# Optimization experiments

Measured on AMD Instinct MI355X. Metric: run time of the kernel, lower is better.

The kernel has to match this reference:

```python
import jax, jax.numpy as jnp
import numpy as np

B, T, DIN, E, H, P = 8, 2048, 256, 256, 4, 8
HD = E // H


def _xavier(key, out_dim, in_dim):
    lim = float(np.sqrt(6.0 / (in_dim + out_dim)))
    return jax.random.uniform(key, (out_dim, in_dim), jnp.float32, -lim, lim)


def setup_inputs() -> dict:
    key = jax.random.key(0)
    ks = jax.random.split(key, 9)
    return {
        "x": jax.random.normal(ks[0], (B, T, DIN), jnp.float32),
        "w_in": _xavier(ks[1], E, DIN), "b_in": jnp.zeros((E,), jnp.float32),
        # MHA in-projections (torch packs qkv; xavier over packed [3E,E] approximated per-slice)
        "w_q": _xavier(ks[2], E, E), "b_q": jnp.zeros((E,), jnp.float32),
        "w_k": _xavier(ks[3], E, E), "b_k": jnp.zeros((E,), jnp.float32),
        "w_v": _xavier(ks[4], E, E), "b_v": jnp.zeros((E,), jnp.float32),
        "w_o": _xavier(ks[5], E, E), "b_o": jnp.zeros((E,), jnp.float32),
        "w_bd": _xavier(ks[6], 1, E), "b_bd": jnp.zeros((1,), jnp.float32),
        "w_pr": _xavier(ks[7], E, E), "b_pr": jnp.zeros((E,), jnp.float32),
    }


def reference(x, w_in, b_in, w_q, b_q, w_k, b_k, w_v, b_v, w_o, b_o, w_bd, b_bd, w_pr, b_pr):
    b, t, _ = x.shape
    h = x @ w_in.T + b_in                                   # [B,T,E]
    # self-attention (batch_first MHA, eval mode -> dropout is identity)
    q = (h @ w_q.T + b_q).reshape(b, t, H, HD)
    k = (h @ w_k.T + b_k).reshape(b, t, H, HD)
    v = (h @ w_v.T + b_v).reshape(b, t, H, HD)
    scale = 1.0 / np.sqrt(HD).astype(np.float32)
    scores = jnp.einsum("bqhd,bkhd->bhqk", q * scale, k)   # [B,H,T,T]
    attn = jax.nn.softmax(scores, axis=-1)
    ao = jnp.einsum("bhqk,bkhd->bqhd", attn, v).reshape(b, t, E)
    ao = ao @ w_o.T + b_o
    # boundary scoring -> dynamic patch ids
    bs = jax.nn.sigmoid(ao @ w_bd.T + b_bd)[..., 0]         # [B,T]
    cum = jnp.cumsum(bs, axis=1)
    normalized = cum / jnp.maximum(cum[:, -1:], 1e-6)
    pid = jnp.minimum((normalized * P).astype(jnp.int32), P - 1)  # [B,T]
    # mean-pool h into P dynamic patches (scatter_add + counts, via one-hot segment matmul)
    oh = jax.nn.one_hot(pid, P, dtype=h.dtype)              # [B,T,P]
    patch_emb = jnp.einsum("btp,btd->bpd", oh, h)           # [B,P,E]
    counts = oh.sum(axis=1)[..., None]                      # [B,P,1]
    patch_emb = patch_emb / jnp.maximum(counts, 1.0)
    return patch_emb @ w_pr.T + b_pr                        # [B,P,E]
```

## Files before the change

kernel.cpp:

```cpp
#include <hip/hip_runtime.h>
#include <cstddef>

#define NB 8
#define NT 2048
#define NE 256
#define NH 4
#define ND 64
#define NP 8

typedef short bf16x8 __attribute__((ext_vector_type(8)));
typedef float f32x4 __attribute__((ext_vector_type(4)));

__device__ __forceinline__ unsigned short f2bf(float f) {
  unsigned u = __builtin_bit_cast(unsigned, f);
  u += 0x7fffu + ((u >> 16) & 1u);
  return (unsigned short)(u >> 16);
}
__device__ __forceinline__ float bf2f(unsigned short h) {
  unsigned u = ((unsigned)h) << 16;
  return __builtin_bit_cast(float, u);
}
__device__ __forceinline__ void split2(float a, float b, unsigned& hi, unsigned& lo) {
  const unsigned short ha = f2bf(a), hb = f2bf(b);
  hi = (unsigned)ha | ((unsigned)hb << 16);
  const unsigned short la = f2bf(a - bf2f(ha));
  const unsigned short lb = f2bf(b - bf2f(hb));
  lo = (unsigned)la | ((unsigned)lb << 16);
}
__device__ __forceinline__ void gld16(const void* g, void* l) {
  __builtin_amdgcn_global_load_lds((const __attribute__((address_space(1))) unsigned*)g,
                                   (__attribute__((address_space(3))) unsigned*)l, 16, 0, 0);
}

__global__ __launch_bounds__(256) void setup_kernel(
    const float* __restrict__ w_in, const float* __restrict__ w_q,
    const float* __restrict__ w_k, const float* __restrict__ b_q,
    const float* __restrict__ b_k, const float* __restrict__ w_o,
    const float* __restrict__ b_o, const float* __restrict__ w_bd,
    const float* __restrict__ b_bd, const float* __restrict__ w_v,
    const float* __restrict__ b_v,
    unsigned short* __restrict__ wihi, unsigned short* __restrict__ wilo,
    unsigned short* __restrict__ wqkvhi, unsigned short* __restrict__ wqkvlo,
    float* __restrict__ bqk, float* __restrict__ consts, float* __restrict__ psum)
{
  __shared__ float wbd_s[NE];
  __shared__ float u_s[NE];
  const int b = blockIdx.x, tid = threadIdx.x;
  if (b < 512) {
    const int i = b * 256 + tid;
    const float v = (i < 65536) ? w_q[i] * 0.125f : w_k[i - 65536];
    const unsigned short h = f2bf(v);
    wqkvhi[i] = h;
    wqkvlo[i] = f2bf(v - bf2f(h));
    if (i < 512) bqk[i] = (i < 256) ? b_q[i] * 0.125f : b_k[i - 256];
  } else if (b < 576) {
    const int i = (b - 512) * 256 + tid;
    const float4 v = *(const float4*)(w_in + (size_t)i * 4);
    const float vv[4] = {v.x, v.y, v.z, v.w};
    unsigned short h4[4], l4[4];
    #pragma unroll
    for (int j = 0; j < 4; ++j) {
      h4[j] = f2bf(vv[j]);
      l4[j] = f2bf(vv[j] - bf2f(h4[j]));
    }
    *(ushort2*)(wihi + (size_t)i * 4)     = make_ushort2(h4[0], h4[1]);
    *(ushort2*)(wihi + (size_t)i * 4 + 2) = make_ushort2(h4[2], h4[3]);
    *(ushort2*)(wilo + (size_t)i * 4)     = make_ushort2(l4[0], l4[1]);
    *(ushort2*)(wilo + (size_t)i * 4 + 2) = make_ushort2(l4[2], l4[3]);
  } else if (b == 576) {
    wbd_s[tid] = w_bd[tid];
    __syncthreads();
    float a = 0.f;
    for (int j = 0; j < NE; ++j) a = fmaf(wbd_s[j], w_o[j * NE + tid], a);
    u_s[tid] = a;
    __syncthreads();
    #pragma unroll
    for (int hh = 0; hh < NH; ++hh) {
      float a2 = 0.f;
      for (int d = 0; d < ND; ++d)
        a2 = fmaf(u_s[hh * ND + d], w_v[(size_t)(hh * ND + d) * NE + tid], a2);
      const unsigned short hb = f2bf(a2);
      wqkvhi[(512 + hh) * 256 + tid] = hb;
      wqkvlo[(512 + hh) * 256 + tid] = f2bf(a2 - bf2f(hb));
    }
    for (int i = tid; i < 60 * 256; i += 256) {
      wqkvhi[516 * 256 + i] = 0;
      wqkvlo[516 * 256 + i] = 0;
    }
    if (tid == 0) {
      float cc = 0.f;
      for (int j = 0; j < NE; ++j) cc = fmaf(wbd_s[j], b_o[j], cc);
      consts[0] = cc + b_bd[0];
    }
    if (tid < 4) {
      float cv = 0.f;
      for (int d = 0; d < ND; ++d) cv = fmaf(u_s[tid * ND + d], b_v[tid * ND + d], cv);
      bqk[512 + tid] = cv;
    } else if (tid < 64) {
      bqk[512 + tid] = 0.f;
    }
  } else {
    for (int i = tid; i < NB * NP * NE; i += 256) psum[i] = 0.f;
  }
}

__global__ __launch_bounds__(256) void hgemm_kernel(
    const float* __restrict__ x,
    const unsigned short* __restrict__ wihi, const unsigned short* __restrict__ wilo,
    const float* __restrict__ b_in,
    unsigned short* __restrict__ hhi, unsigned short* __restrict__ hlo)
{
  __shared__ __align__(16) char sm[2][24576];
  const int tid = threadIdx.x;
  const int wave = tid >> 6, lane = tid & 63;
  const int lr = lane & 15, lg = lane >> 4;
  const int wm = wave >> 1, wn = wave & 1;
  const int bid = blockIdx.x;
  const int idx = bid >> 3;
  const int m0 = ((bid & 7) * 16 + (idx >> 2)) * 128;
  const int n0 = (idx & 3) * 64;

  const float* aSrc[4];
  #pragma unroll
  for (int c = 0; c < 4; ++c) {
    const int L = c * 4096 + tid * 16;
    const int row = L >> 7, w = (L >> 4) & 7;
    aSrc[c] = x + (size_t)(m0 + row) * 256 + (w ^ (row & 7)) * 4;
  }
  const unsigned short* wSrc[2];
  #pragma unroll
  for (int c = 0; c < 2; ++c) {
    const int L = c * 4096 + tid * 16;
    const int half = (L >> 12) & 1;
    const int Lh = L & 4095;
    const int col = Lh >> 6, w = (Lh >> 4) & 3;
    wSrc[c] = (half ? wilo : wihi) + (size_t)(n0 + col) * 256 + (w ^ ((col >> 1) & 3)) * 8;
  }
  int aoff[4][2], woff[2];
  #pragma unroll
  for (int s = 0; s < 4; ++s) {
    const int row = wm * 64 + s * 16 + lr;
    const int b0 = row * 128 + lg * 32;
    const int f = (row & 7) << 4;
    aoff[s][0] = b0 ^ f;
    aoff[s][1] = (b0 + 16) ^ f;
  }
  #pragma unroll
  for (int ns = 0; ns < 2; ++ns) {
    const int col = wn * 32 + ns * 16 + lr;
    woff[ns] = (col * 64 + lg * 16) ^ (((col >> 1) & 3) << 4);
  }

  f32x4 acc[4][2];
  #pragma unroll
  for (int s = 0; s < 4; ++s)
    #pragma unroll
    for (int ns = 0; ns < 2; ++ns) acc[s][ns] = (f32x4){0.f, 0.f, 0.f, 0.f};

  {
    char* lb = sm[0];
    #pragma unroll
    for (int c = 0; c < 4; ++c) gld16(aSrc[c], lb + c * 4096 + wave * 1024);
    #pragma unroll
    for (int c = 0; c < 2; ++c) gld16(wSrc[c], lb + 16384 + c * 4096 + wave * 1024);
  }

  for (int kt = 0; kt < 8; ++kt) {
    __syncthreads();
    if (kt < 7) {
      char* nb = sm[(kt + 1) & 1];
      #pragma unroll
      for (int c = 0; c < 4; ++c) gld16(aSrc[c] + (kt + 1) * 32, nb + c * 4096 + wave * 1024);
      #pragma unroll
      for (int c = 0; c < 2; ++c) gld16(wSrc[c] + (kt + 1) * 32, nb + 16384 + c * 4096 + wave * 1024);
    }
    const char* lb = sm[kt & 1];
    bf16x8 ah[4], al[4], wh[2], wl[2];
    #pragma unroll
    for (int s = 0; s < 4; ++s) {
      const f32x4 p0 = *(const f32x4*)(lb + aoff[s][0]);
      const f32x4 p1 = *(const f32x4*)(lb + aoff[s][1]);
      unsigned h0, h1, h2, h3, l0, l1, l2, l3;
      split2(p0[0], p0[1], h0, l0);
      split2(p0[2], p0[3], h1, l1);
      split2(p1[0], p1[1], h2, l2);
      split2(p1[2], p1[3], h3, l3);
      const uint4 hu = make_uint4(h0, h1, h2, h3);
      const uint4 lu = make_uint4(l0, l1, l2, l3);
      ah[s] = __builtin_bit_cast(bf16x8, hu);
      al[s] = __builtin_bit_cast(bf16x8, lu);
    }
    #pragma unroll
    for (int ns = 0; ns < 2; ++ns) {
      wh[ns] = *(const bf16x8*)(lb + 16384 + woff[ns]);
      wl[ns] = *(const bf16x8*)(lb + 20480 + woff[ns]);
    }
    #pragma unroll
    for (int s = 0; s < 4; ++s)
      #pragma unroll
      for (int ns = 0; ns < 2; ++ns) {
        acc[s][ns] = __builtin_amdgcn_mfma_f32_16x16x32_bf16(ah[s], wh[ns], acc[s][ns], 0, 0, 0);
        acc[s][ns] = __builtin_amdgcn_mfma_f32_16x16x32_bf16(ah[s], wl[ns], acc[s][ns], 0, 0, 0);
        acc[s][ns] = __builtin_amdgcn_mfma_f32_16x16x32_bf16(al[s], wh[ns], acc[s][ns], 0, 0, 0);
      }
  }
  #pragma unroll
  for (int s = 0; s < 4; ++s)
    #pragma unroll
    for (int ns = 0; ns < 2; ++ns)
      #pragma unroll
      for (int reg = 0; reg < 4; ++reg) {
        const int row = m0 + wm * 64 + s * 16 + lg * 4 + reg;
        const int col = n0 + wn * 32 + ns * 16 + lr;
        const float v = acc[s][ns][reg] + b_in[col];
        const size_t i2 = (size_t)row * 256 + col;
        const unsigned short hb = f2bf(v);
        hhi[i2] = hb;
        hlo[i2] = f2bf(v - bf2f(hb));
      }
}

__global__ __launch_bounds__(256) void qkvgemm_kernel(
    const unsigned short* __restrict__ Ahi, const unsigned short* __restrict__ Alo,
    const unsigned short* __restrict__ Whi, const unsigned short* __restrict__ Wlo,
    const float* __restrict__ bias,
    unsigned short* __restrict__ Qhi, unsigned short* __restrict__ Qlo,
    unsigned short* __restrict__ Khi, unsigned short* __restrict__ Klo,
    float* __restrict__ vubuf)
{
  __shared__ __align__(16) char sm[2][24576];
  const int tid = threadIdx.x;
  const int wave = tid >> 6, lane = tid & 63;
  const int lr = lane & 15, lg = lane >> 4;
  const int wm = wave >> 1, wn = wave & 1;
  const int bid = blockIdx.x;
  const int idx = bid >> 3;
  const int m0 = ((bid & 7) * 16 + idx / 9) * 128;
  const int n0 = (idx % 9) * 64;

  const unsigned short* aSrc[4];
  #pragma unroll
  for (int c = 0; c < 4; ++c) {
    const int L = c * 4096 + tid * 16;
    const int half = L >> 13;
    const int Lh = L & 8191;
    const int row = Lh >> 6, w = (Lh >> 4) & 3;
    aSrc[c] = (half ? Alo : Ahi) + (size_t)(m0 + row) * 256 + (w ^ ((row >> 1) & 3)) * 8;
  }
  const unsigned short* wSrc[2];
  #pragma unroll
  for (int c = 0; c < 2; ++c) {
    const int L = c * 4096 + tid * 16;
    const int half = (L >> 12) & 1;
    const int Lh = L & 4095;
    const int col = Lh >> 6, w = (Lh >> 4) & 3;
    wSrc[c] = (half ? Wlo : Whi) + (size_t)(n0 + col) * 256 + (w ^ ((col >> 1) & 3)) * 8;
  }
  int aoff[4], woff[2];
  #pragma unroll
  for (int s = 0; s < 4; ++s) {
    const int row = wm * 64 + s * 16 + lr;
    aoff[s] = (row * 64 + lg * 16) ^ (((row >> 1) & 3) << 4);
  }
  #pragma unroll
  for (int ns = 0; ns < 2; ++ns) {
    const int col = wn * 32 + ns * 16 + lr;
    woff[ns] = (col * 64 + lg * 16) ^ (((col >> 1) & 3) << 4);
  }

  f32x4 acc[4][2];
  #pragma unroll
  for (int s = 0; s < 4; ++s)
    #pragma unroll
    for (int ns = 0; ns < 2; ++ns) acc[s][ns] = (f32x4){0.f, 0.f, 0.f, 0.f};

  {
    char* lb = sm[0];
    #pragma unroll
    for (int c = 0; c < 4; ++c) gld16(aSrc[c], lb + c * 4096 + wave * 1024);
    #pragma unroll
    for (int c = 0; c < 2; ++c) gld16(wSrc[c], lb + 16384 + c * 4096 + wave * 1024);
  }

  for (int kt = 0; kt < 8; ++kt) {
    __syncthreads();
    if (kt < 7) {
      char* nb = sm[(kt + 1) & 1];
      #pragma unroll
      for (int c = 0; c < 4; ++c) gld16(aSrc[c] + (kt + 1) * 32, nb + c * 4096 + wave * 1024);
      #pragma unroll
      for (int c = 0; c < 2; ++c) gld16(wSrc[c] + (kt + 1) * 32, nb + 16384 + c * 4096 + wave * 1024);
    }
    const char* lb = sm[kt & 1];
    bf16x8 ah[4], al[4], wh[2], wl[2];
    #pragma unroll
    for (int s = 0; s < 4; ++s) {
      ah[s] = *(const bf16x8*)(lb + aoff[s]);
      al[s] = *(const bf16x8*)(lb + 8192 + aoff[s]);
    }
    #pragma unroll
    for (int ns = 0; ns < 2; ++ns) {
      wh[ns] = *(const bf16x8*)(lb + 16384 + woff[ns]);
      wl[ns] = *(const bf16x8*)(lb + 20480 + woff[ns]);
    }
    #pragma unroll
    for (int s = 0; s < 4; ++s)
      #pragma unroll
      for (int ns = 0; ns < 2; ++ns) {
        acc[s][ns] = __builtin_amdgcn_mfma_f32_16x16x32_bf16(ah[s], wh[ns], acc[s][ns], 0, 0, 0);
        acc[s][ns] = __builtin_amdgcn_mfma_f32_16x16x32_bf16(ah[s], wl[ns], acc[s][ns], 0, 0, 0);
        acc[s][ns] = __builtin_amdgcn_mfma_f32_16x16x32_bf16(al[s], wh[ns], acc[s][ns], 0, 0, 0);
      }
  }
  #pragma unroll
  for (int s = 0; s < 4; ++s)
    #pragma unroll
    for (int ns = 0; ns < 2; ++ns)
      #pragma unroll
      for (int reg = 0; reg < 4; ++reg) {
        const int row = m0 + wm * 64 + s * 16 + lg * 4 + reg;
        const int col = n0 + wn * 32 + ns * 16 + lr;
        const float v = acc[s][ns][reg] + bias[col];
        const int b = row >> 11, t = row & 2047;
        if (col < 512) {
          const int c = col & 255;
          const int head = c >> 6, d = c & 63;
          const size_t i2 = (((size_t)(b * NH + head)) * NT + t) * ND + d;
          const unsigned short hb = f2bf(v);
          if (col < 256) { Qhi[i2] = hb; Qlo[i2] = f2bf(v - bf2f(hb)); }
          else           { Khi[i2] = hb; Klo[i2] = f2bf(v - bf2f(hb)); }
        } else if (col < 516) {
          vubuf[((size_t)(b * NH + (col - 512))) * NT + t] = v;
        }
      }
}

__global__ __launch_bounds__(512) void attn_kernel5(
    const unsigned short* __restrict__ qhi, const unsigned short* __restrict__ qlo,
    const unsigned short* __restrict__ khi, const unsigned short* __restrict__ klo,
    const float* __restrict__ vu, float2* __restrict__ part2)
{
  __shared__ __align__(16) char kbuf[2][16384];
  __shared__ float vu_s[512];
  const int tid = threadIdx.x;
  const int wave = tid >> 6, lane = tid & 63;
  const int lr = lane & 15, lg = lane >> 4;
  const int bid = blockIdx.x;
  const int g = bid >> 3;
  const int bh = (bid & 7) * 4 + (g >> 5);
  const int rem = g & 31;
  const int qt = rem >> 2, kh = rem & 3;
  const size_t base = (size_t)bh * NT * ND;
  const int qrow0 = qt * 256 + wave * 32;
  const int krow0 = kh * 512;

  vu_s[tid] = vu[(size_t)bh * NT + krow0 + tid];

  bf16x8 qf[2][2][2];
  #pragma unroll
  for (int s = 0; s < 2; ++s)
    #pragma unroll
    for (int ds = 0; ds < 2; ++ds) {
      const size_t off = base + (size_t)(qrow0 + s * 16 + lr) * ND + ds * 32 + lg * 8;
      qf[s][ds][0] = *(const bf16x8*)(qhi + off);
      qf[s][ds][1] = *(const bf16x8*)(qlo + off);
    }

  const int so = (tid * 16) ^ (((tid >> 3) & 7) << 4);
  int ro0[4], ro1[4];
  #pragma unroll
  for (int ns = 0; ns < 4; ++ns) {
    const int r = ns * 16 + lr;
    const int sw = (r & 7) << 4;
    const int ob = r * 128 + lg * 16;
    ro0[ns] = ob ^ sw;
    ro1[ns] = (ob + 64) ^ sw;
  }
  const char* srcH = (const char*)(khi + base + (size_t)krow0 * ND);
  const char* srcL = (const char*)(klo + base + (size_t)krow0 * ND);
  gld16(srcH + so, &kbuf[0][wave * 1024]);
  gld16(srcL + so, &kbuf[0][8192 + wave * 1024]);

  float l[8], sv[8];
  #pragma unroll
  for (int i = 0; i < 8; ++i) { l[i] = 0.f; sv[i] = 0.f; }

  #pragma unroll 2
  for (int kt = 0; kt < 8; ++kt) {
    __syncthreads();
    if (kt < 7) {
      char* nb = kbuf[(kt + 1) & 1];
      gld16(srcH + (kt + 1) * 8192 + so, nb + wave * 1024);
      gld16(srcL + (kt + 1) * 8192 + so, nb + 8192 + wave * 1024);
    }
    const char* kb = (const char*)kbuf[kt & 1];
    f32x4 acc[2][4];
    float vuv[4];
    #pragma unroll
    for (int ns = 0; ns < 4; ++ns) {
      const bf16x8 kh0 = *(const bf16x8*)(kb + ro0[ns]);
      const bf16x8 kh1 = *(const bf16x8*)(kb + ro1[ns]);
      const bf16x8 kl0 = *(const bf16x8*)(kb + 8192 + ro0[ns]);
      const bf16x8 kl1 = *(const bf16x8*)(kb + 8192 + ro1[ns]);
      vuv[ns] = vu_s[kt * 64 + ns * 16 + lr];
      #pragma unroll
      for (int s = 0; s < 2; ++s) {
        acc[s][ns] = (f32x4){0.f, 0.f, 0.f, 0.f};
        acc[s][ns] = __builtin_amdgcn_mfma_f32_16x16x32_bf16(qf[s][0][0], kh0, acc[s][ns], 0, 0, 0);
        acc[s][ns] = __builtin_amdgcn_mfma_f32_16x16x32_bf16(qf[s][0][0], kl0, acc[s][ns], 0, 0, 0);
        acc[s][ns] = __builtin_amdgcn_mfma_f32_16x16x32_bf16(qf[s][0][1], kh0, acc[s][ns], 0, 0, 0);
        acc[s][ns] = __builtin_amdgcn_mfma_f32_16x16x32_bf16(qf[s][1][0], kh1, acc[s][ns], 0, 0, 0);
        acc[s][ns] = __builtin_amdgcn_mfma_f32_16x16x32_bf16(qf[s][1][0], kl1, acc[s][ns], 0, 0, 0);
        acc[s][ns] = __builtin_amdgcn_mfma_f32_16x16x32_bf16(qf[s][1][1], kh1, acc[s][ns], 0, 0, 0);
      }
    }
    #pragma unroll
    for (int s = 0; s < 2; ++s)
      #pragma unroll
      for (int reg = 0; reg < 4; ++reg) {
        const int ri = s * 4 + reg;
        #pragma unroll
        for (int ns = 0; ns < 4; ++ns) {
          const float e = __expf(acc[s][ns][reg]);
          l[ri] += e;
          sv[ri] = fmaf(e, vuv[ns], sv[ri]);
        }
      }
  }
  #pragma unroll
  for (int ri = 0; ri < 8; ++ri) {
    #pragma unroll
    for (int off = 1; off < 16; off <<= 1) {
      l[ri]  += __shfl_xor(l[ri],  off, 16);
      sv[ri] += __shfl_xor(sv[ri], off, 16);
    }
  }
  if (lr == 0) {
    #pragma unroll
    for (int s = 0; s < 2; ++s)
      #pragma unroll
      for (int reg = 0; reg < 4; ++reg) {
        const int row = qrow0 + s * 16 + lg * 4 + reg;
        part2[(((size_t)bh * NT + row) << 2) + kh] = make_float2(l[s * 4 + reg], sv[s * 4 + reg]);
      }
  }
}

__global__ __launch_bounds__(256) void boundary_kernel(
    const float4* __restrict__ part4, const float* __restrict__ consts,
    int* __restrict__ pid, int* __restrict__ counts)
{
  const int b = blockIdx.x, tid = threadIdx.x;
  __shared__ float partial[256];
  __shared__ int cnt_s[8];
  const float c = consts[0];
  float v[8];
  float run = 0.f;
  #pragma unroll
  for (int i = 0; i < 8; ++i) {
    const int t = tid * 8 + i;
    float logit = c;
    #pragma unroll
    for (int hh = 0; hh < NH; ++hh) {
      const size_t p0 = ((size_t)(b * NH + hh) * NT + t) * 2;
      const float4 a = part4[p0];
      const float4 d = part4[p0 + 1];
      logit += (a.y + a.w + d.y + d.w) / (a.x + a.z + d.x + d.z);
    }
    const float bs = 1.f / (1.f + expf(-logit));
    run += bs;
    v[i] = run;
  }
  float x = run;
  partial[tid] = x;
  __syncthreads();
  for (int off = 1; off < 256; off <<= 1) {
    const float y = (tid >= off) ? partial[tid - off] : 0.f;
    __syncthreads();
    x += y;
    partial[tid] = x;
    __syncthreads();
  }
  const float total = partial[255];
  if (tid < 8) cnt_s[tid] = 0;
  __syncthreads();
  const float denom = fmaxf(total, 1e-6f);
  const float excl = x - run;
  #pragma unroll
  for (int i = 0; i < 8; ++i) {
    const float norm = (excl + v[i]) / denom;
    int pp = (int)(norm * 8.f);
    pp = pp > 7 ? 7 : pp;
    pid[b * NT + tid * 8 + i] = pp;
    atomicAdd(&cnt_s[pp], 1);
  }
  __syncthreads();
  if (tid < 8) counts[b * 8 + tid] = cnt_s[tid];
}

__global__ __launch_bounds__(256) void pool_kernel(
    const unsigned short* __restrict__ hhi, const int* __restrict__ pid,
    float* __restrict__ psum)
{
  const int b = blockIdx.x >> 4, chunk = blockIdx.x & 15;
  const int tid = threadIdx.x;
  __shared__ int pid_s[128];
  const int t0 = chunk * 128;
  if (tid < 128) pid_s[tid] = pid[b * NT + t0 + tid];
  __syncthreads();
  float acc[8] = {};
  for (int tok = 0; tok < 128; ++tok) {
    const float val = bf2f(hhi[((size_t)b * NT + t0 + tok) * NE + tid]);
    const int p = pid_s[tok];
    #pragma unroll
    for (int pp = 0; pp < 8; ++pp) acc[pp] += (p == pp) ? val : 0.f;
  }
  #pragma unroll
  for (int pp = 0; pp < 8; ++pp)
    atomicAdd(&psum[((size_t)b * NP + pp) * NE + tid], acc[pp]);
}

__global__ __launch_bounds__(256) void final_kernel(
    const float* __restrict__ psum, const int* __restrict__ counts,
    const float* __restrict__ w_pr, const float* __restrict__ b_pr, float* __restrict__ out)
{
  const int bp = blockIdx.x;
  const int tid = threadIdx.x;
  __shared__ float pe[NE];
  const float cnt = fmaxf((float)counts[bp], 1.f);
  pe[tid] = psum[(size_t)bp * NE + tid] / cnt;
  __syncthreads();
  float acc = 0.f;
  for (int e = 0; e < NE; ++e) acc = fmaf(pe[e], w_pr[(size_t)tid * NE + e], acc);
  out[(size_t)bp * NE + tid] = acc + b_pr[tid];
}

extern "C" void kernel_launch(void* const* d_in, const int* in_sizes, int n_in,
                              void* d_out, int out_size, void* d_ws, size_t ws_size,
                              hipStream_t stream) {
  (void)in_sizes; (void)n_in; (void)out_size; (void)ws_size;
  const float* x    = (const float*)d_in[0];
  const float* w_in = (const float*)d_in[1];
  const float* b_in = (const float*)d_in[2];
  const float* w_q  = (const float*)d_in[3];
  const float* b_q  = (const float*)d_in[4];
  const float* w_k  = (const float*)d_in[5];
  const float* b_k  = (const float*)d_in[6];
  const float* w_v  = (const float*)d_in[7];
  const float* b_v  = (const float*)d_in[8];
  const float* w_o  = (const float*)d_in[9];
  const float* b_o  = (const float*)d_in[10];
  const float* w_bd = (const float*)d_in[11];
  const float* b_bd = (const float*)d_in[12];
  const float* w_pr = (const float*)d_in[13];
  const float* b_pr = (const float*)d_in[14];
  float* out = (float*)d_out;

  const size_t M = (size_t)NB * NT;
  unsigned short* hhi = (unsigned short*)d_ws;
  unsigned short* hlo = hhi + M * NE;
  unsigned short* qhi = hlo + M * NE;
  unsigned short* qlo = qhi + M * NE;
  unsigned short* khi = qlo + M * NE;
  unsigned short* klo = khi + M * NE;
  unsigned short* wihi = klo + M * NE;
  unsigned short* wilo = wihi + 65536;
  unsigned short* wqkvhi = wilo + 65536;
  unsigned short* wqkvlo = wqkvhi + 147456;
  float* bqk    = (float*)(wqkvlo + 147456);
  float* vubuf  = bqk + 576;
  float* part   = vubuf + 65536;
  float* consts = part + 524288;
  float* psum   = consts + 8;
  int*   pid    = (int*)(psum + 16384);
  int*   counts = pid + 16384;

  setup_kernel<<<578, 256, 0, stream>>>(w_in, w_q, w_k, b_q, b_k, w_o, b_o,
      w_bd, b_bd, w_v, b_v, wihi, wilo, wqkvhi, wqkvlo, bqk, consts, psum);
  hgemm_kernel<<<512, 256, 0, stream>>>(x, wihi, wilo, b_in, hhi, hlo);
  qkvgemm_kernel<<<1152, 256, 0, stream>>>(hhi, hlo, wqkvhi, wqkvlo, bqk,
      qhi, qlo, khi, klo, vubuf);
  attn_kernel5<<<1024, 512, 0, stream>>>(qhi, qlo, khi, klo, vubuf, (float2*)part);
  boundary_kernel<<<8, 256, 0, stream>>>((const float4*)part, consts, pid, counts);
  pool_kernel<<<128, 256, 0, stream>>>(hhi, pid, psum);
  final_kernel<<<64, 256, 0, stream>>>(psum, counts, w_pr, b_pr, out);
}
```

Baseline: 157.9 us.

## Split attention keys into eight chunks, prefetch all K tiles, use exp2

The attention kernel now splits the key dimension into 8 chunks of 256 instead of 4 chunks of 512, doubling the grid to 2048 blocks. Each block loads all four K tiles into LDS up front, with one barrier, instead of double-buffering with a barrier per step. The Q scale folds in log2(e) so the softmax can use the hardware exp2 instruction, and the MFMA section is wrapped in setprio. The boundary kernel reduces 8 partials per row instead of 4. This costs 64KB LDS per block, which may limit occupancy, and doubles the partial-sum traffic.

```diff
diff --git a/kernel.cpp b/kernel.cpp
--- a/kernel.cpp
+++ b/kernel.cpp
@@ -31,6 +31,8 @@
   __builtin_amdgcn_global_load_lds((const __attribute__((address_space(1))) unsigned*)g,
                                    (__attribute__((address_space(3))) unsigned*)l, 16, 0, 0);
 }
+
+#define QSC 0.180336880111120419f
 
 __global__ __launch_bounds__(256) void setup_kernel(
     const float* __restrict__ w_in, const float* __restrict__ w_q,
@@ -48,11 +50,11 @@
   const int b = blockIdx.x, tid = threadIdx.x;
   if (b < 512) {
     const int i = b * 256 + tid;
-    const float v = (i < 65536) ? w_q[i] * 0.125f : w_k[i - 65536];
+    const float v = (i < 65536) ? w_q[i] * QSC : w_k[i - 65536];
     const unsigned short h = f2bf(v);
     wqkvhi[i] = h;
     wqkvlo[i] = f2bf(v - bf2f(h));
-    if (i < 512) bqk[i] = (i < 256) ? b_q[i] * 0.125f : b_k[i - 256];
+    if (i < 512) bqk[i] = (i < 256) ? b_q[i] * QSC : b_k[i - 256];
   } else if (b < 576) {
     const int i = (b - 512) * 256 + tid;
     const float4 v = *(const float4*)(w_in + (size_t)i * 4);
@@ -335,26 +337,26 @@
       }
 }
 
-__global__ __launch_bounds__(512) void attn_kernel5(
+__global__ __launch_bounds__(512) void attn_kernel6(
     const unsigned short* __restrict__ qhi, const unsigned short* __restrict__ qlo,
     const unsigned short* __restrict__ khi, const unsigned short* __restrict__ klo,
     const float* __restrict__ vu, float2* __restrict__ part2)
 {
-  __shared__ __align__(16) char kbuf[2][16384];
-  __shared__ float vu_s[512];
+  __shared__ __align__(16) char kbuf[4][16384];
+  __shared__ float vu_s[256];
   const int tid = threadIdx.x;
   const int wave = tid >> 6, lane = tid & 63;
   const int lr = lane & 15, lg = lane >> 4;
   const int bid = blockIdx.x;
-  const int g = bid >> 3;
-  const int bh = (bid & 7) * 4 + (g >> 5);
-  const int rem = g & 31;
-  const int qt = rem >> 2, kh = rem & 3;
+  const int idx = bid >> 3;
+  const int bh = (bid & 7) * 4 + (idx >> 6);
+  const int rem = idx & 63;
+  const int qt = rem >> 3, kh = rem & 7;
   const size_t base = (size_t)bh * NT * ND;
   const int qrow0 = qt * 256 + wave * 32;
-  const int krow0 = kh * 512;
-
-  vu_s[tid] = vu[(size_t)bh * NT + krow0 + tid];
+  const int krow0 = kh * 256;
+
+  if (tid < 256) vu_s[tid] = vu[(size_t)bh * NT + krow0 + tid];
 
   bf16x8 qf[2][2][2];
   #pragma unroll
@@ -378,24 +380,23 @@
   }
   const char* srcH = (const char*)(khi + base + (size_t)krow0 * ND);
   const char* srcL = (const char*)(klo + base + (size_t)krow0 * ND);
-  gld16(srcH + so, &kbuf[0][wave * 1024]);
-  gld16(srcL + so, &kbuf[0][8192 + wave * 1024]);
+  #pragma unroll
+  for (int t = 0; t < 4; ++t) {
+    gld16(srcH + t * 8192 + so, &kbuf[t][wave * 1024]);
+    gld16(srcL + t * 8192 + so, &kbuf[t][8192 + wave * 1024]);
+  }
+  __syncthreads();
 
   float l[8], sv[8];
   #pragma unroll
   for (int i = 0; i < 8; ++i) { l[i] = 0.f; sv[i] = 0.f; }
 
   #pragma unroll 2
-  for (int kt = 0; kt < 8; ++kt) {
-    __syncthreads();
-    if (kt < 7) {
-      char* nb = kbuf[(kt + 1) & 1];
-      gld16(srcH + (kt + 1) * 8192 + so, nb + wave * 1024);
-      gld16(srcL + (kt + 1) * 8192 + so, nb + 8192 + wave * 1024);
-    }
-    const char* kb = (const char*)kbuf[kt & 1];
+  for (int kt = 0; kt < 4; ++kt) {
+    const char* kb = (const char*)kbuf[kt];
     f32x4 acc[2][4];
     float vuv[4];
+    __builtin_amdgcn_s_setprio(1);
     #pragma unroll
     for (int ns = 0; ns < 4; ++ns) {
       const bf16x8 kh0 = *(const bf16x8*)(kb + ro0[ns]);
@@ -414,6 +415,7 @@
         acc[s][ns] = __builtin_amdgcn_mfma_f32_16x16x32_bf16(qf[s][1][1], kh1, acc[s][ns], 0, 0, 0);
       }
     }
+    __builtin_amdgcn_s_setprio(0);
     #pragma unroll
     for (int s = 0; s < 2; ++s)
       #pragma unroll
@@ -421,7 +423,7 @@
         const int ri = s * 4 + reg;
         #pragma unroll
         for (int ns = 0; ns < 4; ++ns) {
-          const float e = __expf(acc[s][ns][reg]);
+          const float e = __builtin_amdgcn_exp2f(acc[s][ns][reg]);
           l[ri] += e;
           sv[ri] = fmaf(e, vuv[ns], sv[ri]);
         }
@@ -441,7 +443,7 @@
       #pragma unroll
       for (int reg = 0; reg < 4; ++reg) {
         const int row = qrow0 + s * 16 + lg * 4 + reg;
-        part2[(((size_t)bh * NT + row) << 2) + kh] = make_float2(l[s * 4 + reg], sv[s * 4 + reg]);
+        part2[(((size_t)bh * NT + row) << 3) + kh] = make_float2(l[s * 4 + reg], sv[s * 4 + reg]);
       }
   }
 }
@@ -462,10 +464,15 @@
     float logit = c;
     #pragma unroll
     for (int hh = 0; hh < NH; ++hh) {
-      const size_t p0 = ((size_t)(b * NH + hh) * NT + t) * 2;
-      const float4 a = part4[p0];
-      const float4 d = part4[p0 + 1];
-      logit += (a.y + a.w + d.y + d.w) / (a.x + a.z + d.x + d.z);
+      const size_t p0 = ((size_t)(b * NH + hh) * NT + t) * 4;
+      float lsum = 0.f, ssum = 0.f;
+      #pragma unroll
+      for (int q = 0; q < 4; ++q) {
+        const float4 p = part4[p0 + q];
+        lsum += p.x + p.z;
+        ssum += p.y + p.w;
+      }
+      logit += ssum / lsum;
     }
     const float bs = 1.f / (1.f + expf(-logit));
     run += bs;
@@ -570,7 +577,7 @@
   float* bqk    = (float*)(wqkvlo + 147456);
   float* vubuf  = bqk + 576;
   float* part   = vubuf + 65536;
-  float* consts = part + 524288;
+  float* consts = part + 1048576;
   float* psum   = consts + 8;
   int*   pid    = (int*)(psum + 16384);
   int*   counts = pid + 16384;
@@ -580,7 +587,7 @@
   hgemm_kernel<<<512, 256, 0, stream>>>(x, wihi, wilo, b_in, hhi, hlo);
   qkvgemm_kernel<<<1152, 256, 0, stream>>>(hhi, hlo, wqkvhi, wqkvlo, bqk,
       qhi, qlo, khi, klo, vubuf);
-  attn_kernel5<<<1024, 512, 0, stream>>>(qhi, qlo, khi, klo, vubuf, (float2*)part);
+  attn_kernel6<<<2048, 512, 0, stream>>>(qhi, qlo, khi, klo, vubuf, (float2*)part);
   boundary_kernel<<<8, 256, 0, stream>>>((const float4*)part, consts, pid, counts);
   pool_kernel<<<128, 256, 0, stream>>>(hhi, pid, psum);
   final_kernel<<<64, 256, 0, stream>>>(psum, counts, w_pr, b_pr, out);
```

After: 166.4 us. +5.4%, slower.
